# Kernel optimization log

Hardware: AMD Instinct MI355X
Metric: run time of the kernel (lower is better)

## Reference

```python
import jax, jax.numpy as jnp
import numpy as np

HID, NH_FULL, K, GAMMA = 768, 12, 9, 2
HD = HID // NH_FULL            # 64
NH = NH_FULL // GAMMA          # 6
RH = HD * NH                   # 384 reduced hidden dim
OUT_HALF = HID // 2            # 384
B, S = 8, 1024


def setup_inputs() -> dict:
    key0 = jax.random.key(0)
    ks = jax.random.split(key0, 20)
    r = lambda i, shape, sc=0.02: (jax.random.normal(ks[i], shape, dtype=jnp.float32) * sc)
    inp = {
        'query': jax.random.normal(ks[0], (B, S, HID), dtype=jnp.float32),
        'mask': jnp.ones((B, 1, 1, S), dtype=jnp.int32),
        # q/k/v projections: hidden -> reduced
        'Wq': r(1, (HID, RH)), 'bq': jnp.zeros((RH,), jnp.float32),
        'Wk': r(2, (HID, RH)), 'bk': jnp.zeros((RH,), jnp.float32),
        'Wv': r(3, (HID, RH)), 'bv': jnp.zeros((RH,), jnp.float32),
        # depthwise separable conv: depthwise [HID,1,K] + pointwise [RH,HID]
        'dw_w': r(4, (HID, 1, K), 0.1), 'dw_b': jnp.zeros((HID,), jnp.float32),
        'pw_w': r(5, (RH, HID)), 'pw_b': jnp.zeros((RH,), jnp.float32),
        # self-attn output proj: reduced -> hidden//2
        'Wsa': r(6, (RH, OUT_HALF)), 'bsa': jnp.zeros((OUT_HALF,), jnp.float32),
        # dynamic kernel layer: reduced -> K*NH
        'Wdk': r(7, (RH, K * NH)), 'bdk': jnp.zeros((K * NH,), jnp.float32),
        # dynamic attn output proj: reduced -> hidden//2
        'Wda': r(8, (RH, OUT_HALF)), 'bda': jnp.zeros((OUT_HALF,), jnp.float32),
    }
    # self_attn=True requires query==key==value
    inp['key'] = inp['query']
    inp['value'] = inp['query']
    return inp


def _forward(query, key, value, mask, Wq, bq, Wk, bk, Wv, bv,
             dw_w, dw_b, pw_w, pw_b, Wsa, bsa, Wdk, bdk, Wda, bda):
    b, s, _ = query.shape
    q = query @ Wq + bq          # [B,S,RH]
    k = key @ Wk + bk
    v = value @ Wv + bv

    # ---- depthwise separable conv over key (seq axis), 'same' padding ----
    key_t = jnp.transpose(key, (0, 2, 1))  # [B,HID,S]
    dw = jax.lax.conv_general_dilated(
        key_t, dw_w, window_strides=(1,), padding=[(K // 2, K // 2)],
        feature_group_count=HID, dimension_numbers=('NCH', 'OIH', 'NCH'))
    dw = dw + dw_b[None, :, None]          # [B,HID,S]
    ks_feat = jnp.einsum('bhs,rh->bsr', dw, pw_w) + pw_b  # [B,S,RH]

    # ---- standard multi-head self-attention branch ----
    def split(x):  # [B,S,RH] -> [B,NH,S,HD]
        return x.reshape(b, s, NH, HD).transpose(0, 2, 1, 3)
    qh, kh, vh = split(q), split(k), split(v)
    scores = jnp.einsum('bhqd,bhkd->bhqk', qh, kh) / jnp.sqrt(jnp.float32(HD))
    scores = jnp.where(mask == 0, jnp.float32(-jnp.inf), scores)
    attn_wts = jax.nn.softmax(scores, axis=-1)             # [B,NH,S,S]
    attn_out = jnp.einsum('bhqk,bhkd->bhqd', attn_wts, vh)
    attn_out = attn_out.transpose(0, 2, 1, 3).reshape(b, s, RH)
    self_out = attn_out @ Wsa + bsa                         # [B,S,HID//2]

    # ---- span dynamic conv attention branch ----
    # unfold v into sliding windows: expanded[b,s,h,d,k] = v_pad[b, s+k, h*HD+d]
    v_pad = jnp.pad(v, ((0, 0), (K // 2, K // 2), (0, 0)))  # [B,S+K-1,RH]
    windows = jnp.stack([v_pad[:, i:i + s] for i in range(K)], axis=-1)  # [B,S,RH,K]
    windows = windows.reshape(b, s, NH, HD, K)
    dyn_logits = (q * ks_feat) @ Wdk + bdk                  # [B,S,K*NH]
    dyn_kernel = jax.nn.softmax(dyn_logits.reshape(b, s, NH, K), axis=-1)
    dyn_out = jnp.einsum('bshdk,bshk->bshd', windows, dyn_kernel).reshape(b, s, RH)
    dyn_out = dyn_out @ Wda + bda                           # [B,S,HID//2]

    return attn_wts, jnp.concatenate([self_out, dyn_out], axis=-1)


def reference(query, key, value, mask, Wq, bq, Wk, bk, Wv, bv,
              dw_w, dw_b, pw_w, pw_b, Wsa, bsa, Wdk, bdk, Wda, bda):
    return _forward(query, key, value, mask, Wq, bq, Wk, bk, Wv, bv,
                    dw_w, dw_b, pw_w, pw_b, Wsa, bsa, Wdk, bdk, Wda, bda)
```

## Files before the change

kernel.cpp:

```cpp
#include <hip/hip_runtime.h>
#include <math.h>

#define B 8
#define S 1024
#define HID 768
#define RH 384
#define NH 6
#define HD 64
#define KW 9
#define KNH 54
#define OUTHALF 384
#define QLD 1152

typedef __attribute__((ext_vector_type(8))) short short8;
typedef __attribute__((ext_vector_type(4))) float f32x4;

#define SWZ(r, c) (((r) << 6) + ((c) ^ (((r) & 7) << 3)))

__device__ __forceinline__ ushort f2bf(float x) {
    unsigned u = __float_as_uint(x);
    u += 0x7FFF + ((u >> 16) & 1);
    return (ushort)(u >> 16);
}
__device__ __forceinline__ float bf2f(ushort u) {
    return __uint_as_float(((unsigned)u) << 16);
}
__device__ __forceinline__ short8 cvt8(const float* p) {
    short8 r;
    #pragma unroll
    for (int i = 0; i < 8; i++) r[i] = (short)f2bf(p[i]);
    return r;
}

__global__ __launch_bounds__(256) void cvt_bf16(const float* __restrict__ in,
                                                ushort* __restrict__ out, int n8)
{
    int i = blockIdx.x*256 + threadIdx.x;
    if (i >= n8) return;
    float buf[8];
    *(float4*)&buf[0] = *(const float4*)(in + i*8);
    *(float4*)&buf[4] = *(const float4*)(in + i*8 + 4);
    *(short8*)(out + i*8) = cvt8(buf);
}

__global__ __launch_bounds__(256) void prep_weights(
    const float* __restrict__ Wq, const float* __restrict__ Wk, const float* __restrict__ Wv,
    const float* __restrict__ bq, const float* __restrict__ bk, const float* __restrict__ bv,
    const float* __restrict__ pw_w, const float* __restrict__ Wsa,
    const float* __restrict__ Wda, const float* __restrict__ Wdk,
    ushort* __restrict__ WqkvT, ushort* __restrict__ pw_bf,
    ushort* __restrict__ WsaT, ushort* __restrict__ WdaT, ushort* __restrict__ WdkT,
    float* __restrict__ bqkv)
{
    int i = blockIdx.x*256 + threadIdx.x;
    if (i < 884736) {
        int n = i / 768, kk = i % 768;
        int w = n / 384, nn = n % 384;
        const float* W = (w == 0) ? Wq : (w == 1) ? Wk : Wv;
        WqkvT[i] = f2bf(W[kk*384 + nn]);
        return;
    }
    i -= 884736;
    if (i < 294912) { pw_bf[i] = f2bf(pw_w[i]); return; }
    i -= 294912;
    if (i < 147456) {
        int n = i / 384, kk = i % 384;
        WsaT[i] = f2bf(Wsa[kk*384 + n]);
        return;
    }
    i -= 147456;
    if (i < 147456) {
        int n = i / 384, kk = i % 384;
        WdaT[i] = f2bf(Wda[kk*384 + n]);
        return;
    }
    i -= 147456;
    if (i < 49152) {
        int n = i / 384, kk = i % 384;
        WdkT[i] = (n < KNH) ? f2bf(Wdk[kk*KNH + n]) : (ushort)0;
        return;
    }
    i -= 49152;
    if (i < 1152) {
        bqkv[i] = (i < 384) ? bq[i] : (i < 768) ? bk[i-384] : bv[i-768];
    }
}

template<bool OUTBF>
__global__ __launch_bounds__(256) void gemm_mfma(
    const ushort* __restrict__ A, const ushort* __restrict__ Bt,
    const float* __restrict__ bias, void* __restrict__ Cout,
    int N, int Kd, int ldc)
{
    __shared__ __attribute__((aligned(16))) ushort As[128*32];
    __shared__ __attribute__((aligned(16))) ushort Bs[128*32];
    const int t = threadIdx.x;
    const int wave = t >> 6, lane = t & 63;
    const int lr = lane & 15, lg = lane >> 4;
    const int wr = wave >> 1, wc = wave & 1;
    const int bm = blockIdx.y * 128, bn = blockIdx.x * 128;

    f32x4 acc[4][4] = {};
    const int srow = t >> 1, sseg = t & 1;
    const ushort* Arow = A + (size_t)(bm + srow)*Kd + sseg*16;
    const ushort* Brow = Bt + (size_t)(bn + srow)*Kd + sseg*16;
    const int g0 = (sseg*2) ^ (srow & 3), g1 = (sseg*2 + 1) ^ (srow & 3);
    const int swz = lg ^ (lr & 3);

    for (int k0 = 0; k0 < Kd; k0 += 32) {
        short8 av0 = *(const short8*)(Arow + k0);
        short8 av1 = *(const short8*)(Arow + k0 + 8);
        short8 bv0 = *(const short8*)(Brow + k0);
        short8 bv1 = *(const short8*)(Brow + k0 + 8);
        __syncthreads();
        *(short8*)&As[srow*32 + g0*8] = av0;
        *(short8*)&As[srow*32 + g1*8] = av1;
        *(short8*)&Bs[srow*32 + g0*8] = bv0;
        *(short8*)&Bs[srow*32 + g1*8] = bv1;
        __syncthreads();
        short8 af[4], bfr[4];
        #pragma unroll
        for (int m = 0; m < 4; m++)
            af[m] = *(const short8*)&As[(wr*64 + m*16 + lr)*32 + swz*8];
        #pragma unroll
        for (int n = 0; n < 4; n++)
            bfr[n] = *(const short8*)&Bs[(wc*64 + n*16 + lr)*32 + swz*8];
        #pragma unroll
        for (int m = 0; m < 4; m++)
            #pragma unroll
            for (int n = 0; n < 4; n++)
                acc[m][n] = __builtin_amdgcn_mfma_f32_16x16x32_bf16(af[m], bfr[n], acc[m][n], 0, 0, 0);
    }

    #pragma unroll
    for (int m = 0; m < 4; m++) {
        #pragma unroll
        for (int n = 0; n < 4; n++) {
            int gcol = bn + wc*64 + n*16 + lr;
            if (gcol >= N) continue;
            float bz = bias[gcol];
            #pragma unroll
            for (int r = 0; r < 4; r++) {
                size_t grow = bm + wr*64 + m*16 + lg*4 + r;
                float val = acc[m][n][r] + bz;
                if (OUTBF) ((ushort*)Cout)[grow*ldc + gcol] = f2bf(val);
                else       ((float*)Cout)[grow*ldc + gcol] = val;
            }
        }
    }
}

__global__ __launch_bounds__(256) void attn_fused(
    const ushort* __restrict__ qkv, const int* __restrict__ mask,
    float* __restrict__ out0, ushort* __restrict__ attnws)
{
    __shared__ __attribute__((aligned(16))) ushort Ks[64*64];
    __shared__ __attribute__((aligned(16))) ushort Vt[64*64];
    __shared__ __attribute__((aligned(16))) ushort Ps[4][16*64];

    const int b = blockIdx.z, h = blockIdx.y, q0 = blockIdx.x * 64;
    const int t = threadIdx.x;
    const int wave = t >> 6, lane = t & 63;
    const int lr = lane & 15, lg = lane >> 4;

    const ushort* qrow = qkv + (size_t)(b*S + q0 + wave*16 + lr)*QLD + h*HD;
    short8 aQ0 = *(const short8*)(qrow + lg*8);
    short8 aQ1 = *(const short8*)(qrow + 32 + lg*8);

    const int srow = t >> 2;
    const int sseg = t & 3;
    const int* mrow = mask + b*S;
    const ushort* kbase = qkv + RH;
    const ushort* vbase = qkv + 2*RH;

    float lsum[4] = {0.f, 0.f, 0.f, 0.f};

    for (int kc = 0; kc < S; kc += 64) {
        const ushort* kr = kbase + (size_t)(b*S + kc + srow)*QLD + h*HD + sseg*16;
        short8 kv0 = *(const short8*)(kr);
        short8 kv1 = *(const short8*)(kr + 8);
        __syncthreads();
        *(short8*)&Ks[SWZ(srow, sseg*16)]     = kv0;
        *(short8*)&Ks[SWZ(srow, sseg*16 + 8)] = kv1;
        __syncthreads();
        #pragma unroll
        for (int t4 = 0; t4 < 4; t4++) {
            short8 b0 = *(const short8*)&Ks[SWZ(t4*16 + lr, lg*8)];
            short8 b1 = *(const short8*)&Ks[SWZ(t4*16 + lr, 32 + lg*8)];
            f32x4 c = {0.f, 0.f, 0.f, 0.f};
            c = __builtin_amdgcn_mfma_f32_16x16x32_bf16(aQ0, b0, c, 0, 0, 0);
            c = __builtin_amdgcn_mfma_f32_16x16x32_bf16(aQ1, b1, c, 0, 0, 0);
            float add = mrow[kc + t4*16 + lr] ? 0.f : -1e30f;
            #pragma unroll
            for (int r = 0; r < 4; r++)
                lsum[r] += __expf(c[r]*0.125f + add);
        }
    }
    #pragma unroll
    for (int r = 0; r < 4; r++) {
        #pragma unroll
        for (int off = 1; off < 16; off <<= 1)
            lsum[r] += __shfl_xor(lsum[r], off, 16);
    }
    float inv[4];
    #pragma unroll
    for (int r = 0; r < 4; r++) inv[r] = 1.f / lsum[r];

    f32x4 o[4] = {};
    ushort* Psw = &Ps[wave][0];
    const size_t obase = ((size_t)((b*NH + h)*S) + q0 + wave*16) * (size_t)S;

    for (int kc = 0; kc < S; kc += 64) {
        const ushort* kr = kbase + (size_t)(b*S + kc + srow)*QLD + h*HD + sseg*16;
        short8 kv0 = *(const short8*)(kr);
        short8 kv1 = *(const short8*)(kr + 8);
        ushort vb[16];
        #pragma unroll
        for (int i = 0; i < 16; i++)
            vb[i] = vbase[(size_t)(b*S + kc + sseg*16 + i)*QLD + h*HD + srow];
        __syncthreads();
        *(short8*)&Ks[SWZ(srow, sseg*16)]     = kv0;
        *(short8*)&Ks[SWZ(srow, sseg*16 + 8)] = kv1;
        *(short8*)&Vt[SWZ(srow, sseg*16)]     = *(short8*)&vb[0];
        *(short8*)&Vt[SWZ(srow, sseg*16 + 8)] = *(short8*)&vb[8];
        __syncthreads();

        #pragma unroll
        for (int t4 = 0; t4 < 4; t4++) {
            short8 b0 = *(const short8*)&Ks[SWZ(t4*16 + lr, lg*8)];
            short8 b1 = *(const short8*)&Ks[SWZ(t4*16 + lr, 32 + lg*8)];
            f32x4 c = {0.f, 0.f, 0.f, 0.f};
            c = __builtin_amdgcn_mfma_f32_16x16x32_bf16(aQ0, b0, c, 0, 0, 0);
            c = __builtin_amdgcn_mfma_f32_16x16x32_bf16(aQ1, b1, c, 0, 0, 0);
            float add = mrow[kc + t4*16 + lr] ? 0.f : -1e30f;
            #pragma unroll
            for (int r = 0; r < 4; r++) {
                float p = __expf(c[r]*0.125f + add) * inv[r];
                out0[obase + (size_t)(lg*4 + r)*S + kc + t4*16 + lr] = p;
                Psw[SWZ(lg*4 + r, t4*16 + lr)] = f2bf(p);
            }
        }
        #pragma unroll
        for (int kh = 0; kh < 2; kh++) {
            short8 pa = *(const short8*)&Psw[SWZ(lr, kh*32 + lg*8)];
            #pragma unroll
            for (int dt = 0; dt < 4; dt++) {
                short8 vv = *(const short8*)&Vt[SWZ(dt*16 + lr, kh*32 + lg*8)];
                o[dt] = __builtin_amdgcn_mfma_f32_16x16x32_bf16(pa, vv, o[dt], 0, 0, 0);
            }
        }
    }

    #pragma unroll
    for (int dt = 0; dt < 4; dt++)
        #pragma unroll
        for (int r = 0; r < 4; r++)
            attnws[(size_t)(b*S + q0 + wave*16 + lg*4 + r)*RH + h*HD + dt*16 + lr] = f2bf(o[dt][r]);
}

__global__ __launch_bounds__(256) void dwconv_kernel(
    const float* __restrict__ key, const float* __restrict__ dw_w,
    const float* __restrict__ dw_b, ushort* __restrict__ dwout)
{
    int idx = blockIdx.x*256 + threadIdx.x;
    if (idx >= B*S*(HID/4)) return;
    int h4 = (idx % (HID/4))*4;
    int s  = (idx / (HID/4)) % S;
    int b  = idx / ((HID/4)*S);
    float4 acc = *(const float4*)(dw_b + h4);
    #pragma unroll
    for (int kk = 0; kk < KW; kk++) {
        int sp = s + kk - KW/2;
        if (sp >= 0 && sp < S) {
            float4 kv = *(const float4*)(key + ((size_t)b*S + sp)*HID + h4);
            acc.x += kv.x * dw_w[(h4+0)*KW + kk];
            acc.y += kv.y * dw_w[(h4+1)*KW + kk];
            acc.z += kv.z * dw_w[(h4+2)*KW + kk];
            acc.w += kv.w * dw_w[(h4+3)*KW + kk];
        }
    }
    ushort4 o;
    o.x = f2bf(acc.x); o.y = f2bf(acc.y); o.z = f2bf(acc.z); o.w = f2bf(acc.w);
    *(ushort4*)(dwout + ((size_t)b*S + s)*HID + h4) = o;
}

__global__ __launch_bounds__(256) void qks_kernel(
    const ushort* __restrict__ qkv, const float* __restrict__ ksf,
    ushort* __restrict__ outb)
{
    int i = blockIdx.x*256 + threadIdx.x;
    if (i >= B*S*(RH/8)) return;
    int row = i / (RH/8);
    int c0 = (i % (RH/8))*8;
    short8 qv = *(const short8*)(qkv + (size_t)row*QLD + c0);
    float kf[8];
    *(float4*)&kf[0] = *(const float4*)(ksf + (size_t)row*RH + c0);
    *(float4*)&kf[4] = *(const float4*)(ksf + (size_t)row*RH + c0 + 4);
    short8 o;
    #pragma unroll
    for (int j = 0; j < 8; j++)
        o[j] = (short)f2bf(bf2f((ushort)qv[j]) * kf[j]);
    *(short8*)(outb + (size_t)row*RH + c0) = o;
}

__global__ __launch_bounds__(256) void dyn_conv(
    const float* __restrict__ logits, const ushort* __restrict__ qkv,
    ushort* __restrict__ dynout)
{
    int idx = blockIdx.x*256 + threadIdx.x;
    if (idx >= B*S*(RH/4)) return;
    int r4 = (idx % (RH/4))*4;
    int s  = (idx / (RH/4)) % S;
    int b  = idx / ((RH/4)*S);
    int h  = r4 / HD;
    const float* lg = logits + ((size_t)b*S + s)*KNH + h*KW;
    float mx = lg[0];
    #pragma unroll
    for (int kk = 1; kk < KW; kk++) mx = fmaxf(mx, lg[kk]);
    float e[KW], sum = 0.f;
    #pragma unroll
    for (int kk = 0; kk < KW; kk++) { e[kk] = __expf(lg[kk]-mx); sum += e[kk]; }
    float inv = 1.f/sum;
    float acc[4] = {0.f, 0.f, 0.f, 0.f};
    const ushort* vbase = qkv + 2*RH;
    #pragma unroll
    for (int kk = 0; kk < KW; kk++) {
        int sp = s + kk - KW/2;
        if (sp >= 0 && sp < S) {
            const ushort* vp = vbase + (size_t)(b*S + sp)*QLD + r4;
            #pragma unroll
            for (int j = 0; j < 4; j++) acc[j] += bf2f(vp[j]) * e[kk];
        }
    }
    ushort4 o;
    o.x = f2bf(acc[0]*inv); o.y = f2bf(acc[1]*inv);
    o.z = f2bf(acc[2]*inv); o.w = f2bf(acc[3]*inv);
    *(ushort4*)(dynout + ((size_t)b*S + s)*RH + r4) = o;
}

extern "C" void kernel_launch(void* const* d_in, const int* in_sizes, int n_in,
                              void* d_out, int out_size, void* d_ws, size_t ws_size,
                              hipStream_t stream) {
    const float* query = (const float*)d_in[0];
    const int*   mask  = (const int*)d_in[1];
    const float* Wq    = (const float*)d_in[2];
    const float* bq    = (const float*)d_in[3];
    const float* Wk    = (const float*)d_in[4];
    const float* bk    = (const float*)d_in[5];
    const float* Wv    = (const float*)d_in[6];
    const float* bv    = (const float*)d_in[7];
    const float* dw_w  = (const float*)d_in[8];
    const float* dw_b  = (const float*)d_in[9];
    const float* pw_w  = (const float*)d_in[10];
    const float* pw_b  = (const float*)d_in[11];
    const float* Wsa   = (const float*)d_in[12];
    const float* bsa   = (const float*)d_in[13];
    const float* Wdk   = (const float*)d_in[14];
    const float* bdk   = (const float*)d_in[15];
    const float* Wda   = (const float*)d_in[16];
    const float* bda   = (const float*)d_in[17];

    float* out0 = (float*)d_out;
    float* out1 = out0 + (size_t)B*NH*S*S;

    char* wsb = (char*)d_ws;
    size_t off = 0;
    auto alloc = [&](size_t bytes) { char* p = wsb + off; off += (bytes + 255) & ~255ull; return p; };
    ushort* Xbf    = (ushort*)alloc((size_t)B*S*HID*2);
    ushort* qkvbf  = (ushort*)alloc((size_t)B*S*QLD*2);
    ushort* dwbf   = (ushort*)alloc((size_t)B*S*HID*2);
    float*  ksf    = (float*) alloc((size_t)B*S*RH*4);
    ushort* attnbf = (ushort*)alloc((size_t)B*S*RH*2);
    ushort* qksbf  = (ushort*)alloc((size_t)B*S*RH*2);
    ushort* dynbf  = (ushort*)alloc((size_t)B*S*RH*2);
    float*  dynlog = (float*) alloc((size_t)B*S*KNH*4);
    ushort* WqkvT  = (ushort*)alloc((size_t)QLD*HID*2);
    ushort* pw_bf  = (ushort*)alloc((size_t)RH*HID*2);
    ushort* WsaT   = (ushort*)alloc((size_t)RH*RH*2);
    ushort* WdaT   = (ushort*)alloc((size_t)RH*RH*2);
    ushort* WdkT   = (ushort*)alloc((size_t)128*RH*2);
    float*  bqkv   = (float*) alloc((size_t)QLD*4);

    const int M = B*S;

    cvt_bf16<<<(M*HID/8 + 255)/256, 256, 0, stream>>>(query, Xbf, M*HID/8);
    prep_weights<<<(1524864 + 255)/256, 256, 0, stream>>>(
        Wq, Wk, Wv, bq, bk, bv, pw_w, Wsa, Wda, Wdk,
        WqkvT, pw_bf, WsaT, WdaT, WdkT, bqkv);

    gemm_mfma<true><<<dim3(QLD/128, M/128), 256, 0, stream>>>(
        Xbf, WqkvT, bqkv, qkvbf, QLD, HID, QLD);

    dwconv_kernel<<<(M*(HID/4) + 255)/256, 256, 0, stream>>>(query, dw_w, dw_b, dwbf);
    gemm_mfma<false><<<dim3(RH/128, M/128), 256, 0, stream>>>(
        dwbf, pw_bf, pw_b, ksf, RH, HID, RH);

    attn_fused<<<dim3(S/64, NH, B), 256, 0, stream>>>(qkvbf, mask, out0, attnbf);

    gemm_mfma<false><<<dim3(RH/128, M/128), 256, 0, stream>>>(
        attnbf, WsaT, bsa, out1, OUTHALF, RH, HID);

    qks_kernel<<<(M*(RH/8) + 255)/256, 256, 0, stream>>>(qkvbf, ksf, qksbf);
    gemm_mfma<false><<<dim3(1, M/128), 256, 0, stream>>>(
        qksbf, WdkT, bdk, dynlog, KNH, RH, KNH);
    dyn_conv<<<(M*(RH/4) + 255)/256, 256, 0, stream>>>(dynlog, qkvbf, dynbf);
    gemm_mfma<false><<<dim3(RH/128, M/128), 256, 0, stream>>>(
        dynbf, WdaT, bda, out1 + OUTHALF, OUTHALF, RH, HID);
}
```

Measured before the change: 323.0 us.

## Fuse small kernels, add 64x64 GEMM for narrow outputs, use exp2 in softmax

Merges the bf16 input conversion with the depthwise conv, fuses the q*ks elementwise product into a dedicated dynamic-kernel logits GEMM, and runs the two output projections as one dual launch of a new 64x64-tile GEMM. The softmax exponent now uses exp2f with a pre-scaled constant. These cut launches and intermediate traffic and give the N=384 GEMMs more blocks, in exchange for a smaller tile with less operand reuse.

Measured after the change: 310.9 us. 3.8% less time.

```diff
diff --git a/kernel.cpp b/kernel.cpp
--- a/kernel.cpp
+++ b/kernel.cpp
@@ -11,6 +11,7 @@
 #define KNH 54
 #define OUTHALF 384
 #define QLD 1152
+#define EXPSCALE 0.18033688f
 
 typedef __attribute__((ext_vector_type(8))) short short8;
 typedef __attribute__((ext_vector_type(4))) float f32x4;
@@ -32,15 +33,38 @@
     return r;
 }
 
-__global__ __launch_bounds__(256) void cvt_bf16(const float* __restrict__ in,
-                                                ushort* __restrict__ out, int n8)
-{
-    int i = blockIdx.x*256 + threadIdx.x;
-    if (i >= n8) return;
-    float buf[8];
-    *(float4*)&buf[0] = *(const float4*)(in + i*8);
-    *(float4*)&buf[4] = *(const float4*)(in + i*8 + 4);
-    *(short8*)(out + i*8) = cvt8(buf);
+__global__ __launch_bounds__(256) void cvt_dw_fused(
+    const float* __restrict__ query, const float* __restrict__ dw_w,
+    const float* __restrict__ dw_b, ushort* __restrict__ Xbf,
+    ushort* __restrict__ dwout)
+{
+    int idx = blockIdx.x*256 + threadIdx.x;
+    if (idx >= B*S*(HID/8)) return;
+    int c0 = (idx % (HID/8))*8;
+    int s  = (idx / (HID/8)) % S;
+    int b  = idx / ((HID/8)*S);
+
+    float ctr[8];
+    *(float4*)&ctr[0] = *(const float4*)(query + ((size_t)b*S + s)*HID + c0);
+    *(float4*)&ctr[4] = *(const float4*)(query + ((size_t)b*S + s)*HID + c0 + 4);
+    *(short8*)(Xbf + ((size_t)b*S + s)*HID + c0) = cvt8(ctr);
+
+    float acc[8];
+    *(float4*)&acc[0] = *(const float4*)(dw_b + c0);
+    *(float4*)&acc[4] = *(const float4*)(dw_b + c0 + 4);
+    #pragma unroll
+    for (int kk = 0; kk < KW; kk++) {
+        int sp = s + kk - KW/2;
+        if (sp >= 0 && sp < S) {
+            float row[8];
+            *(float4*)&row[0] = *(const float4*)(query + ((size_t)b*S + sp)*HID + c0);
+            *(float4*)&row[4] = *(const float4*)(query + ((size_t)b*S + sp)*HID + c0 + 4);
+            #pragma unroll
+            for (int j = 0; j < 8; j++)
+                acc[j] += row[j] * dw_w[(c0+j)*KW + kk];
+        }
+    }
+    *(short8*)(dwout + ((size_t)b*S + s)*HID + c0) = cvt8(acc);
 }
 
 __global__ __launch_bounds__(256) void prep_weights(
@@ -150,6 +174,111 @@
     }
 }
 
+template<bool OUTBF, bool DUAL>
+__global__ __launch_bounds__(256) void gemm64(
+    const ushort* __restrict__ A0, const ushort* __restrict__ Bt0,
+    const float* __restrict__ bias0, void* __restrict__ C0,
+    const ushort* __restrict__ A1, const ushort* __restrict__ Bt1,
+    const float* __restrict__ bias1,
+    int N, int Kd, int ldc)
+{
+    __shared__ __attribute__((aligned(16))) ushort As[64*32];
+    __shared__ __attribute__((aligned(16))) ushort Bs[64*32];
+    const ushort* A  = (DUAL && blockIdx.z) ? A1 : A0;
+    const ushort* Bt = (DUAL && blockIdx.z) ? Bt1 : Bt0;
+    const float* bias = (DUAL && blockIdx.z) ? bias1 : bias0;
+    const int coff = (DUAL && blockIdx.z) ? OUTHALF : 0;
+
+    const int t = threadIdx.x;
+    const int wave = t >> 6, lane = t & 63;
+    const int lr = lane & 15, lg = lane >> 4;
+    const int wr = wave >> 1, wc = wave & 1;
+    const int bm = blockIdx.y * 64, bn = blockIdx.x * 64;
+
+    f32x4 acc[2][2] = {};
+    const int srow = t >> 2, sseg = t & 3;
+    const ushort* Arow = A + (size_t)(bm + srow)*Kd + sseg*8;
+    const ushort* Brow = Bt + (size_t)(bn + srow)*Kd + sseg*8;
+    const int gs = sseg ^ (srow & 3);
+    const int swz = lg ^ (lr & 3);
+
+    for (int k0 = 0; k0 < Kd; k0 += 32) {
+        short8 av = *(const short8*)(Arow + k0);
+        short8 bv = *(const short8*)(Brow + k0);
+        __syncthreads();
+        *(short8*)&As[srow*32 + gs*8] = av;
+        *(short8*)&Bs[srow*32 + gs*8] = bv;
+        __syncthreads();
+        short8 af[2], bfr[2];
+        #pragma unroll
+        for (int m = 0; m < 2; m++)
+            af[m] = *(const short8*)&As[(wr*32 + m*16 + lr)*32 + swz*8];
+        #pragma unroll
+        for (int n = 0; n < 2; n++)
+            bfr[n] = *(const short8*)&Bs[(wc*32 + n*16 + lr)*32 + swz*8];
+        #pragma unroll
+        for (int m = 0; m < 2; m++)
+            #pragma unroll
+            for (int n = 0; n < 2; n++)
+                acc[m][n] = __builtin_amdgcn_mfma_f32_16x16x32_bf16(af[m], bfr[n], acc[m][n], 0, 0, 0);
+    }
+
+    #pragma unroll
+    for (int m = 0; m < 2; m++) {
+        #pragma unroll
+        for (int n = 0; n < 2; n++) {
+            int gcol = bn + wc*32 + n*16 + lr;
+            if (gcol >= N) continue;
+            float bz = bias[gcol];
+            #pragma unroll
+            for (int r = 0; r < 4; r++) {
+                size_t grow = bm + wr*32 + m*16 + lg*4 + r;
+                float val = acc[m][n][r] + bz;
+                if (OUTBF) ((ushort*)C0)[grow*ldc + gcol + coff] = f2bf(val);
+                else       ((float*)C0)[grow*ldc + gcol + coff] = val;
+            }
+        }
+    }
+}
+
+__global__ __launch_bounds__(64) void gemm_qksdk(
+    const ushort* __restrict__ qkv, const float* __restrict__ ksf,
+    const ushort* __restrict__ WdkT, const float* __restrict__ bdk,
+    float* __restrict__ dynlog)
+{
+    const int lane = threadIdx.x;
+    const int lr = lane & 15, lg = lane >> 4;
+    const int r0 = blockIdx.x * 16;
+    const int row = r0 + lr;
+
+    f32x4 acc[4] = {};
+    for (int ks = 0; ks < RH/32; ks++) {
+        int k0 = ks*32 + lg*8;
+        short8 qv = *(const short8*)(qkv + (size_t)row*QLD + k0);
+        float kf[8];
+        *(float4*)&kf[0] = *(const float4*)(ksf + (size_t)row*RH + k0);
+        *(float4*)&kf[4] = *(const float4*)(ksf + (size_t)row*RH + k0 + 4);
+        short8 afr;
+        #pragma unroll
+        for (int j = 0; j < 8; j++)
+            afr[j] = (short)f2bf(bf2f((ushort)qv[j]) * kf[j]);
+        #pragma unroll
+        for (int t4 = 0; t4 < 4; t4++) {
+            short8 bfr = *(const short8*)(WdkT + (size_t)(t4*16 + lr)*RH + k0);
+            acc[t4] = __builtin_amdgcn_mfma_f32_16x16x32_bf16(afr, bfr, acc[t4], 0, 0, 0);
+        }
+    }
+    #pragma unroll
+    for (int t4 = 0; t4 < 4; t4++) {
+        int n = t4*16 + lr;
+        if (n >= KNH) continue;
+        float bz = bdk[n];
+        #pragma unroll
+        for (int r = 0; r < 4; r++)
+            dynlog[(size_t)(r0 + lg*4 + r)*KNH + n] = acc[t4][r] + bz;
+    }
+}
+
 __global__ __launch_bounds__(256) void attn_fused(
     const ushort* __restrict__ qkv, const int* __restrict__ mask,
     float* __restrict__ out0, ushort* __restrict__ attnws)
@@ -193,7 +322,7 @@
             float add = mrow[kc + t4*16 + lr] ? 0.f : -1e30f;
             #pragma unroll
             for (int r = 0; r < 4; r++)
-                lsum[r] += __expf(c[r]*0.125f + add);
+                lsum[r] += exp2f(c[r]*EXPSCALE + add);
         }
     }
     #pragma unroll
@@ -235,7 +364,7 @@
             float add = mrow[kc + t4*16 + lr] ? 0.f : -1e30f;
             #pragma unroll
             for (int r = 0; r < 4; r++) {
-                float p = __expf(c[r]*0.125f + add) * inv[r];
+                float p = exp2f(c[r]*EXPSCALE + add) * inv[r];
                 out0[obase + (size_t)(lg*4 + r)*S + kc + t4*16 + lr] = p;
                 Psw[SWZ(lg*4 + r, t4*16 + lr)] = f2bf(p);
             }
@@ -256,51 +385,6 @@
         #pragma unroll
         for (int r = 0; r < 4; r++)
             attnws[(size_t)(b*S + q0 + wave*16 + lg*4 + r)*RH + h*HD + dt*16 + lr] = f2bf(o[dt][r]);
-}
-
-__global__ __launch_bounds__(256) void dwconv_kernel(
-    const float* __restrict__ key, const float* __restrict__ dw_w,
-    const float* __restrict__ dw_b, ushort* __restrict__ dwout)
-{
-    int idx = blockIdx.x*256 + threadIdx.x;
-    if (idx >= B*S*(HID/4)) return;
-    int h4 = (idx % (HID/4))*4;
-    int s  = (idx / (HID/4)) % S;
-    int b  = idx / ((HID/4)*S);
-    float4 acc = *(const float4*)(dw_b + h4);
-    #pragma unroll
-    for (int kk = 0; kk < KW; kk++) {
-        int sp = s + kk - KW/2;
-        if (sp >= 0 && sp < S) {
-            float4 kv = *(const float4*)(key + ((size_t)b*S + sp)*HID + h4);
-            acc.x += kv.x * dw_w[(h4+0)*KW + kk];
-            acc.y += kv.y * dw_w[(h4+1)*KW + kk];
-            acc.z += kv.z * dw_w[(h4+2)*KW + kk];
-            acc.w += kv.w * dw_w[(h4+3)*KW + kk];
-        }
-    }
-    ushort4 o;
-    o.x = f2bf(acc.x); o.y = f2bf(acc.y); o.z = f2bf(acc.z); o.w = f2bf(acc.w);
-    *(ushort4*)(dwout + ((size_t)b*S + s)*HID + h4) = o;
-}
-
-__global__ __launch_bounds__(256) void qks_kernel(
-    const ushort* __restrict__ qkv, const float* __restrict__ ksf,
-    ushort* __restrict__ outb)
-{
-    int i = blockIdx.x*256 + threadIdx.x;
-    if (i >= B*S*(RH/8)) return;
-    int row = i / (RH/8);
-    int c0 = (i % (RH/8))*8;
-    short8 qv = *(const short8*)(qkv + (size_t)row*QLD + c0);
-    float kf[8];
-    *(float4*)&kf[0] = *(const float4*)(ksf + (size_t)row*RH + c0);
-    *(float4*)&kf[4] = *(const float4*)(ksf + (size_t)row*RH + c0 + 4);
-    short8 o;
-    #pragma unroll
-    for (int j = 0; j < 8; j++)
-        o[j] = (short)f2bf(bf2f((ushort)qv[j]) * kf[j]);
-    *(short8*)(outb + (size_t)row*RH + c0) = o;
 }
 
 __global__ __launch_bounds__(256) void dyn_conv(
@@ -371,7 +455,6 @@
     ushort* dwbf   = (ushort*)alloc((size_t)B*S*HID*2);
     float*  ksf    = (float*) alloc((size_t)B*S*RH*4);
     ushort* attnbf = (ushort*)alloc((size_t)B*S*RH*2);
-    ushort* qksbf  = (ushort*)alloc((size_t)B*S*RH*2);
     ushort* dynbf  = (ushort*)alloc((size_t)B*S*RH*2);
     float*  dynlog = (float*) alloc((size_t)B*S*KNH*4);
     ushort* WqkvT  = (ushort*)alloc((size_t)QLD*HID*2);
@@ -383,27 +466,24 @@
 
     const int M = B*S;
 
-    cvt_bf16<<<(M*HID/8 + 255)/256, 256, 0, stream>>>(query, Xbf, M*HID/8);
     prep_weights<<<(1524864 + 255)/256, 256, 0, stream>>>(
         Wq, Wk, Wv, bq, bk, bv, pw_w, Wsa, Wda, Wdk,
         WqkvT, pw_bf, WsaT, WdaT, WdkT, bqkv);
 
+    cvt_dw_fused<<<(M*(HID/8) + 255)/256, 256, 0, stream>>>(query, dw_w, dw_b, Xbf, dwbf);
+
     gemm_mfma<true><<<dim3(QLD/128, M/128), 256, 0, stream>>>(
         Xbf, WqkvT, bqkv, qkvbf, QLD, HID, QLD);
 
-    dwconv_kernel<<<(M*(HID/4) + 255)/256, 256, 0, stream>>>(query, dw_w, dw_b, dwbf);
-    gemm_mfma<false><<<dim3(RH/128, M/128), 256, 0, stream>>>(
-        dwbf, pw_bf, pw_b, ksf, RH, HID, RH);
+    gemm64<false, false><<<dim3(RH/64, M/64), 256, 0, stream>>>(
+        dwbf, pw_bf, pw_b, ksf, nullptr, nullptr, nullptr, RH, HID, RH);
 
     attn_fused<<<dim3(S/64, NH, B), 256, 0, stream>>>(qkvbf, mask, out0, attnbf);
 
-    gemm_mfma<false><<<dim3(RH/128, M/128), 256, 0, stream>>>(
-        attnbf, WsaT, bsa, out1, OUTHALF, RH, HID);
-
-    qks_kernel<<<(M*(RH/8) + 255)/256, 256, 0, stream>>>(qkvbf, ksf, qksbf);
-    gemm_mfma<false><<<dim3(1, M/128), 256, 0, stream>>>(
-        qksbf, WdkT, bdk, dynlog, KNH, RH, KNH);
+    gemm_qksdk<<<M/16, 64, 0, stream>>>(qkvbf, ksf, WdkT, bdk, dynlog);
+
     dyn_conv<<<(M*(RH/4) + 255)/256, 256, 0, stream>>>(dynlog, qkvbf, dynbf);
-    gemm_mfma<false><<<dim3(RH/128, M/128), 256, 0, stream>>>(
-        dynbf, WdaT, bda, out1 + OUTHALF, OUTHALF, RH, HID);
-}
+
+    gemm64<false, true><<<dim3(OUTHALF/64, M/64, 2), 256, 0, stream>>>(
+        attnbf, WsaT, bsa, out1, dynbf, WdaT, bda, OUTHALF, RH, HID);
+}
```
